# Optimization experiments

Hardware: AMD Instinct MI355X
Metric: run time of the kernel (lower is better)

## Reference

```python
import jax, jax.numpy as jnp
import numpy as np

NUM_HEADS = 8
WS = 2  # window_size


def setup_inputs() -> dict:
    key = jax.random.key(0)
    k1, k2, k3 = jax.random.split(key, 3)
    B, N, C = 8, 4096, 512
    x = jax.random.normal(k1, (B, N, C), dtype=jnp.float32)
    W_qkv = jax.random.normal(k2, (3 * C, C), dtype=jnp.float32) * 0.02  # nn.Linear weight [out,in], no bias
    W_proj = jax.random.normal(k3, (C, C), dtype=jnp.float32) * 0.02
    b_proj = jnp.zeros((C,), dtype=jnp.float32)
    return {"x": x, "W_qkv": W_qkv, "W_proj": W_proj, "b_proj": b_proj}


def _attn(q, k, v, scale):
    # q,k,v: [..., heads, T, hd]
    logits = jnp.einsum('...qd,...kd->...qk', q, k) * scale
    p = jax.nn.softmax(logits, axis=-1)
    return jnp.einsum('...qk,...kd->...qd', p, v)


def reference(x, W_qkv, W_proj, b_proj):
    B, N, C = x.shape
    H = W = int(N ** 0.5)
    nh, hd = NUM_HEADS, C // NUM_HEADS
    scale = hd ** -0.5

    # ---- hi branch: avg-pool then global attention on pooled tokens ----
    x_img = x.reshape(B, H, W, C)
    x_hi = x_img.reshape(B, H // WS, WS, W // WS, WS, C).mean(axis=(2, 4))  # [B,Hh,Wh,C]
    Hh, Wh = H // WS, W // WS
    N_hi = Hh * Wh
    x_hi = x_hi.reshape(B, N_hi, C)

    qkv_hi = (x_hi @ W_qkv.T).reshape(B, N_hi, 3, nh, hd).transpose(2, 0, 3, 1, 4)
    out_hi = _attn(qkv_hi[0], qkv_hi[1], qkv_hi[2], scale)          # [B,nh,N_hi,hd]
    out_hi = out_hi.transpose(0, 2, 1, 3).reshape(B, N_hi, C)

    # bilinear upsample (align_corners=False == half-pixel, matches jax.image.resize)
    hi_img = out_hi.reshape(B, Hh, Wh, C).transpose(0, 3, 1, 2)      # [B,C,Hh,Wh]
    hi_up = jax.image.resize(hi_img, (B, C, H, W), method='bilinear')
    out_hi = hi_up.reshape(B, C, N).transpose(0, 2, 1)               # [B,N,C]

    # ---- lo branch: windowed attention (replicating torch unfold layout) ----
    # torch: x.unfold(1,ws,ws).unfold(2,ws,ws) -> [B,Hh,Wh,C,ws,ws]; then
    # .reshape(B,-1,ws*ws,C) reinterprets the contiguous [C,ws,ws] block as [ws*ws,C].
    wnd = x_img.reshape(B, Hh, WS, Wh, WS, C).transpose(0, 1, 3, 5, 2, 4)  # [B,Hh,Wh,C,ws,ws]
    nW = Hh * Wh
    T = WS * WS
    windows = wnd.reshape(B, nW, T, C)  # same raw-memory reinterpretation as torch

    qkv_lo = (windows @ W_qkv.T).reshape(B, nW, T, 3, nh, hd).transpose(3, 0, 1, 4, 2, 5)
    out_lo = _attn(qkv_lo[0], qkv_lo[1], qkv_lo[2], scale)           # [B,nW,nh,T,hd]
    out_lo = out_lo.transpose(0, 1, 3, 2, 4).reshape(B, nW, T, C)

    out_lo = out_lo.reshape(B, Hh, Wh, WS, WS, C).transpose(0, 1, 3, 2, 4, 5).reshape(B, N, C)

    out = out_hi + out_lo
    out = out @ W_proj.T + b_proj
    return out
```

## Files before the change

kernel.cpp:

```cpp
#include <hip/hip_runtime.h>
#include <stdint.h>

typedef unsigned short u16b;
typedef short s16x8 __attribute__((ext_vector_type(8)));
typedef unsigned short u16x4 __attribute__((ext_vector_type(4)));
typedef float f32x4 __attribute__((ext_vector_type(4)));

__device__ __forceinline__ u16b f2bf(float f) {
    uint32_t u = __float_as_uint(f);
    uint32_t r = (u + 0x7FFFu + ((u >> 16) & 1u)) >> 16;
    return (u16b)r;
}
__device__ __forceinline__ u16b f2bf_fast(float f) {
    return (u16b)((__float_as_uint(f) + 0x8000u) >> 16);
}
__device__ __forceinline__ float bf2f(u16b h) {
    return __uint_as_float(((uint32_t)h) << 16);
}

typedef const __attribute__((address_space(1))) void* gas_ptr;
typedef __attribute__((address_space(3))) void* las_ptr;
__device__ __forceinline__ void gload_lds16(const void* g, void* l) {
    __builtin_amdgcn_global_load_lds((gas_ptr)g, (las_ptr)l, 16, 0, 0);
}

__global__ void cast_weights(const float* __restrict__ wqkv, const float* __restrict__ wproj,
                             u16b* __restrict__ wqkv_bf, u16b* __restrict__ wproj_bf) {
    int i = blockIdx.x * 256 + threadIdx.x;
    if (i < 1536 * 512) wqkv_bf[i] = f2bf(wqkv[i]);
    if (i < 512 * 512) wproj_bf[i] = f2bf(wproj[i]);
}

__global__ __launch_bounds__(256) void pool_pack(const float* __restrict__ x,
                                                 u16b* __restrict__ x_hi,
                                                 u16b* __restrict__ xw) {
    int i = blockIdx.x * 256 + threadIdx.x;
    int c4 = i & 127;
    int t = i >> 7;
    int wj = t & 31, wi = (t >> 5) & 31, b = t >> 10;
    const float* p00 = x + ((size_t)b * 4096 + (size_t)(wi * 2) * 64 + wj * 2) * 512 + c4 * 4;
    f32x4 v00 = *(const f32x4*)p00;
    f32x4 v01 = *(const f32x4*)(p00 + 512);
    f32x4 v10 = *(const f32x4*)(p00 + 64 * 512);
    f32x4 v11 = *(const f32x4*)(p00 + 65 * 512);

    u16b ph[4];
#pragma unroll
    for (int j = 0; j < 4; ++j)
        ph[j] = f2bf((v00[j] + v01[j] + v10[j] + v11[j]) * 0.25f);
    *(u16x4*)(x_hi + (size_t)t * 512 + c4 * 4) = *(u16x4*)ph;

    u16b pk[16];
#pragma unroll
    for (int j = 0; j < 4; ++j) {
        pk[j * 4 + 0] = f2bf(v00[j]);
        pk[j * 4 + 1] = f2bf(v01[j]);
        pk[j * 4 + 2] = f2bf(v10[j]);
        pk[j * 4 + 3] = f2bf(v11[j]);
    }
    u16b* dst = xw + ((size_t)t * 4 + (c4 >> 5)) * 512 + (c4 & 31) * 16;
    *(s16x8*)dst = *(s16x8*)pk;
    *(s16x8*)(dst + 8) = *(s16x8*)(pk + 8);
}

template <int OUT_F32>
__global__ __launch_bounds__(256) void gemm_bt(const u16b* __restrict__ A, const u16b* __restrict__ Bt,
                                               u16b* __restrict__ Cbf, float* __restrict__ Cf,
                                               const float* __restrict__ bias, int M, int Nn, int K) {
    __shared__ u16b As[128 * 64];
    __shared__ u16b Bs[128 * 64];
    int tid = threadIdx.x;
    int wave = tid >> 6, lane = tid & 63;
    int quad = lane >> 4, l15 = lane & 15;
    int m0 = blockIdx.y * 128, n0 = blockIdx.x * 128;
    int wm = (wave >> 1) * 64, wn = (wave & 1) * 64;

    f32x4 acc[4][4] = {};

    int ldrow = lane >> 3;
    int ldk = ((lane & 7) ^ ldrow) * 8;
    int fsw0 = (quad ^ (l15 & 7)) * 8;
    int fsw1 = ((4 + quad) ^ (l15 & 7)) * 8;

    for (int kc = 0; kc < K; kc += 64) {
#pragma unroll
        for (int i = 0; i < 4; ++i) {
            int chunk = wave * 4 + i;
            int row = chunk * 8 + ldrow;
            gload_lds16(A + (size_t)(m0 + row) * K + kc + ldk, As + chunk * 512);
            gload_lds16(Bt + (size_t)(n0 + row) * K + kc + ldk, Bs + chunk * 512);
        }
        __syncthreads();
#pragma unroll
        for (int ks = 0; ks < 2; ++ks) {
            int fo = ks ? fsw1 : fsw0;
            s16x8 a[4], b[4];
#pragma unroll
            for (int mi = 0; mi < 4; ++mi)
                a[mi] = *(const s16x8*)(As + (wm + mi * 16 + l15) * 64 + fo);
#pragma unroll
            for (int ni = 0; ni < 4; ++ni)
                b[ni] = *(const s16x8*)(Bs + (wn + ni * 16 + l15) * 64 + fo);
#pragma unroll
            for (int mi = 0; mi < 4; ++mi)
#pragma unroll
                for (int ni = 0; ni < 4; ++ni)
                    acc[mi][ni] = __builtin_amdgcn_mfma_f32_16x16x32_bf16(a[mi], b[ni], acc[mi][ni], 0, 0, 0);
        }
        __syncthreads();
    }

#pragma unroll
    for (int mi = 0; mi < 4; ++mi)
#pragma unroll
        for (int ni = 0; ni < 4; ++ni) {
            int row = m0 + wm + mi * 16 + quad * 4;
            int col = n0 + wn + ni * 16 + l15;
            if (OUT_F32) {
                float bv = bias[col];
#pragma unroll
                for (int r = 0; r < 4; ++r)
                    Cf[(size_t)(row + r) * Nn + col] = acc[mi][ni][r] + bv;
            } else {
#pragma unroll
                for (int r = 0; r < 4; ++r)
                    Cbf[(size_t)(row + r) * Nn + col] = f2bf(acc[mi][ni][r]);
            }
        }
}

__global__ __launch_bounds__(256) void transpose_v(const u16b* __restrict__ qkv, u16b* __restrict__ vt) {
    __shared__ u16b tile[64 * 72];
    int bh = blockIdx.y, nt = blockIdx.x;
    int b = bh >> 3, h = bh & 7;
    int tid = threadIdx.x;
    int row = tid >> 2, part = tid & 3;
    const u16b* src = qkv + ((size_t)b * 1024 + nt * 64 + row) * 1536 + 1024 + h * 64 + part * 16;
    *(s16x8*)&tile[row * 72 + part * 16] = *(const s16x8*)src;
    *(s16x8*)&tile[row * 72 + part * 16 + 8] = *(const s16x8*)(src + 8);
    __syncthreads();
    u16b* dst = vt + ((size_t)bh * 64 + row) * 1024 + nt * 64 + part * 16;
#pragma unroll
    for (int j = 0; j < 16; ++j) dst[j] = tile[(part * 16 + j) * 72 + row];
}

__global__ __launch_bounds__(256) void attn_hi(const u16b* __restrict__ qkv,
                                               const u16b* __restrict__ vt,
                                               u16b* __restrict__ out_hi) {
    __shared__ u16b Ks[2][64 * 64];
    __shared__ u16b Vs[2][64 * 64];
    __shared__ u16b P[4][16 * 64];
    int tid = threadIdx.x, wave = tid >> 6, lane = tid & 63;
    int quad = lane >> 4, l15 = lane & 15;
    int bh = blockIdx.x;
    int qb = blockIdx.y;
    int b = bh >> 3, h = bh & 7;
    int qr0 = qb * 64 + wave * 16;

    const size_t qkv_b = (size_t)b * 1024 * 1536;
    const u16b* kg = qkv + qkv_b + 512 + h * 64;
    const u16b* vg = vt + (size_t)bh * 64 * 1024;

    int srow8 = lane >> 3;
    int ssw = ((lane & 7) ^ srow8) * 8;
    int fsw0 = (quad ^ (l15 & 7)) * 8;
    int fsw1 = ((4 + quad) ^ (l15 & 7)) * 8;

    s16x8 qf[2];
    qf[0] = *(const s16x8*)(qkv + qkv_b + (size_t)(qr0 + l15) * 1536 + h * 64 + quad * 8);
    qf[1] = *(const s16x8*)(qkv + qkv_b + (size_t)(qr0 + l15) * 1536 + h * 64 + 32 + quad * 8);

#pragma unroll
    for (int i = 0; i < 2; ++i) {
        int chunk = wave * 2 + i;
        int row = chunk * 8 + srow8;
        gload_lds16(kg + (size_t)row * 1536 + ssw, (u16b*)Ks[0] + chunk * 512);
        gload_lds16(vg + (size_t)row * 1024 + ssw, (u16b*)Vs[0] + chunk * 512);
    }

    f32x4 o[4] = {};
    f32x4 ls = {0.f, 0.f, 0.f, 0.f};
    u16b* pl = P[wave];
    const float c_scale = 0.18033688011f;

    for (int kb = 0; kb < 16; ++kb) {
        int cur = kb & 1, nxt = cur ^ 1;
        __syncthreads();
        if (kb < 15) {
#pragma unroll
            for (int i = 0; i < 2; ++i) {
                int chunk = wave * 2 + i;
                int row = chunk * 8 + srow8;
                gload_lds16(kg + (size_t)((kb + 1) * 64 + row) * 1536 + ssw, (u16b*)Ks[nxt] + chunk * 512);
                gload_lds16(vg + (size_t)row * 1024 + (kb + 1) * 64 + ssw, (u16b*)Vs[nxt] + chunk * 512);
            }
        }
        const u16b* Kc = Ks[cur];
        const u16b* Vc = Vs[cur];

        f32x4 s[4] = {};
#pragma unroll
        for (int nt = 0; nt < 4; ++nt) {
            s16x8 kf0 = *(const s16x8*)(Kc + (nt * 16 + l15) * 64 + fsw0);
            s16x8 kf1 = *(const s16x8*)(Kc + (nt * 16 + l15) * 64 + fsw1);
            s[nt] = __builtin_amdgcn_mfma_f32_16x16x32_bf16(qf[0], kf0, s[nt], 0, 0, 0);
            s[nt] = __builtin_amdgcn_mfma_f32_16x16x32_bf16(qf[1], kf1, s[nt], 0, 0, 0);
        }
#pragma unroll
        for (int nt = 0; nt < 4; ++nt) {
            f32x4 p;
#pragma unroll
            for (int r = 0; r < 4; ++r) p[r] = exp2f(s[nt][r] * c_scale);
            ls += p;
#pragma unroll
            for (int r = 0; r < 4; ++r) {
                int prow = quad * 4 + r;
                int slc = (nt * 2 + (l15 >> 3)) ^ (prow & 7);
                pl[prow * 64 + slc * 8 + (l15 & 7)] = f2bf_fast(p[r]);
            }
        }
        s16x8 pa0 = *(const s16x8*)(pl + l15 * 64 + fsw0);
        s16x8 pa1 = *(const s16x8*)(pl + l15 * 64 + fsw1);
#pragma unroll
        for (int nd = 0; nd < 4; ++nd) {
            s16x8 vf0 = *(const s16x8*)(Vc + (nd * 16 + l15) * 64 + fsw0);
            s16x8 vf1 = *(const s16x8*)(Vc + (nd * 16 + l15) * 64 + fsw1);
            o[nd] = __builtin_amdgcn_mfma_f32_16x16x32_bf16(pa0, vf0, o[nd], 0, 0, 0);
            o[nd] = __builtin_amdgcn_mfma_f32_16x16x32_bf16(pa1, vf1, o[nd], 0, 0, 0);
        }
    }

    float rs[4];
#pragma unroll
    for (int r = 0; r < 4; ++r) {
        float t = ls[r];
#pragma unroll
        for (int msk = 1; msk < 16; msk <<= 1) t += __shfl_xor(t, msk);
        rs[r] = 1.f / t;
    }
#pragma unroll
    for (int nd = 0; nd < 4; ++nd)
#pragma unroll
        for (int r = 0; r < 4; ++r) {
            int row = qr0 + quad * 4 + r;
            int col = h * 64 + nd * 16 + l15;
            out_hi[((size_t)b * 1024 + row) * 512 + col] = f2bf(o[nd][r] * rs[r]);
        }
}

__global__ __launch_bounds__(256) void attn_lo_up(const u16b* __restrict__ qkv_lo,
                                                  const u16b* __restrict__ out_hi,
                                                  u16b* __restrict__ attn_sum) {
    int tid = threadIdx.x, wave = tid >> 6, lane = tid & 63;
    int wg = blockIdx.x * 4 + wave;
    int h = wg & 7, w = (wg >> 3) & 1023, b = wg >> 13;
    size_t base = ((size_t)(b * 1024 + w) * 4) * 1536 + h * 64 + lane;
    float q[4], k[4], v[4];
#pragma unroll
    for (int t = 0; t < 4; ++t) {
        q[t] = bf2f(qkv_lo[base + t * 1536]);
        k[t] = bf2f(qkv_lo[base + t * 1536 + 512]);
        v[t] = bf2f(qkv_lo[base + t * 1536 + 1024]);
    }
    float lg[4][4];
#pragma unroll
    for (int tq = 0; tq < 4; ++tq)
#pragma unroll
        for (int tk = 0; tk < 4; ++tk) {
            float d = q[tq] * k[tk];
#pragma unroll
            for (int msk = 1; msk < 64; msk <<= 1) d += __shfl_xor(d, msk);
            lg[tq][tk] = d * 0.125f;
        }
    int wi = w >> 5, wj = w & 31;
    const u16b* hsrc = out_hi + (size_t)b * 1024 * 512 + h * 64 + lane;
#pragma unroll
    for (int tq = 0; tq < 4; ++tq) {
        float mx = fmaxf(fmaxf(lg[tq][0], lg[tq][1]), fmaxf(lg[tq][2], lg[tq][3]));
        float p[4], s = 0.f;
#pragma unroll
        for (int tk = 0; tk < 4; ++tk) { p[tk] = exp2f((lg[tq][tk] - mx) * 1.44269504f); s += p[tk]; }
        float ov = 0.f;
#pragma unroll
        for (int tk = 0; tk < 4; ++tk) ov += p[tk] * v[tk];
        ov /= s;
        int py = tq >> 1, px = tq & 1;
        int y0, y1, x0, x1;
        float wy0, wx0;
        if (py == 0) { y0 = wi > 0 ? wi - 1 : 0; y1 = wi; wy0 = 0.25f; }
        else         { y0 = wi; y1 = wi < 31 ? wi + 1 : 31; wy0 = 0.75f; }
        if (px == 0) { x0 = wj > 0 ? wj - 1 : 0; x1 = wj; wx0 = 0.25f; }
        else         { x0 = wj; x1 = wj < 31 ? wj + 1 : 31; wx0 = 0.75f; }
        float wy1 = 1.f - wy0, wx1 = 1.f - wx0;
        float vu = wy0 * (wx0 * bf2f(hsrc[(size_t)(y0 * 32 + x0) * 512]) + wx1 * bf2f(hsrc[(size_t)(y0 * 32 + x1) * 512]))
                 + wy1 * (wx0 * bf2f(hsrc[(size_t)(y1 * 32 + x0) * 512]) + wx1 * bf2f(hsrc[(size_t)(y1 * 32 + x1) * 512]));
        int n = (wi * 2 + py) * 64 + wj * 2 + px;
        attn_sum[((size_t)b * 4096 + n) * 512 + h * 64 + lane] = f2bf(ov + vu);
    }
}

extern "C" void kernel_launch(void* const* d_in, const int* in_sizes, int n_in,
                              void* d_out, int out_size, void* d_ws, size_t ws_size,
                              hipStream_t stream) {
    (void)in_sizes; (void)n_in; (void)out_size; (void)ws_size;
    const float* x = (const float*)d_in[0];
    const float* Wqkv = (const float*)d_in[1];
    const float* Wproj = (const float*)d_in[2];
    const float* bproj = (const float*)d_in[3];
    float* out = (float*)d_out;

    char* ws = (char*)d_ws;
    size_t off = 0;
    auto alloc = [&](size_t bytes) { void* p = ws + off; off += bytes; return p; };
    u16b* wqkv_bf = (u16b*)alloc((size_t)1536 * 512 * 2);
    u16b* wproj_bf = (u16b*)alloc((size_t)512 * 512 * 2);
    u16b* x_hi    = (u16b*)alloc((size_t)8 * 1024 * 512 * 2);
    u16b* xw      = (u16b*)alloc((size_t)8 * 1024 * 4 * 512 * 2);
    u16b* qkv_hi  = (u16b*)alloc((size_t)8 * 1024 * 1536 * 2);
    u16b* qkv_lo  = (u16b*)alloc((size_t)8 * 4096 * 1536 * 2);
    u16b* vt      = (u16b*)alloc((size_t)64 * 64 * 1024 * 2);
    u16b* out_hi  = (u16b*)alloc((size_t)8 * 1024 * 512 * 2);
    u16b* attn_sum= (u16b*)alloc((size_t)8 * 4096 * 512 * 2);

    cast_weights<<<dim3(3072), dim3(256), 0, stream>>>(Wqkv, Wproj, wqkv_bf, wproj_bf);
    pool_pack<<<dim3(4096), dim3(256), 0, stream>>>(x, x_hi, xw);
    gemm_bt<0><<<dim3(12, 64), dim3(256), 0, stream>>>(x_hi, wqkv_bf, qkv_hi, nullptr, nullptr, 8192, 1536, 512);
    gemm_bt<0><<<dim3(12, 256), dim3(256), 0, stream>>>(xw, wqkv_bf, qkv_lo, nullptr, nullptr, 32768, 1536, 512);
    transpose_v<<<dim3(16, 64), dim3(256), 0, stream>>>(qkv_hi, vt);
    attn_hi<<<dim3(64, 16), dim3(256), 0, stream>>>(qkv_hi, vt, out_hi);
    attn_lo_up<<<dim3(16384), dim3(256), 0, stream>>>(qkv_lo, out_hi, attn_sum);
    gemm_bt<1><<<dim3(4, 256), dim3(256), 0, stream>>>(attn_sum, wproj_bf, nullptr, out, bproj, 32768, 512, 512);
}
```

Baseline: 350.8 us.

## Replace GEMM with 256x256 double-buffered 8-wave pipelined kernel

```diff
diff --git a/kernel.cpp b/kernel.cpp
--- a/kernel.cpp
+++ b/kernel.cpp
@@ -63,59 +63,154 @@
     *(s16x8*)(dst + 8) = *(s16x8*)(pk + 8);
 }
 
+
+template <int RT>
+__device__ __forceinline__ void stage_region(const u16b* gsrc, int K, u16b* lds,
+                                             int wv, int ldrow, int ldk) {
+#pragma unroll
+    for (int j = 0; j < 2; ++j) {
+        int c = j * 8 + wv;
+        int chunk;
+        if (RT == 0)      chunk = c + ((c >> 3) << 3);
+        else if (RT == 1) chunk = c + ((c >> 3) << 3) + 8;
+        else if (RT == 2) chunk = ((c >> 2) << 3) + (c & 3);
+        else              chunk = ((c >> 2) << 3) + (c & 3) + 4;
+        gload_lds16(gsrc + (size_t)(chunk * 8 + ldrow) * K + ldk, lds + chunk * 512);
+    }
+}
+
+template <int MH, int NH, int LOADB>
+__device__ __forceinline__ void ds_quad(const u16b* Asb, const u16b* Bsb,
+                                        int gm, int gn, int l15, int fsw0, int fsw1,
+                                        s16x8 (&af)[4][2], s16x8 (&bf)[2][2]) {
+#pragma unroll
+    for (int i = 0; i < 4; ++i) {
+        const u16b* p = Asb + (gm * 128 + (MH * 4 + i) * 16 + l15) * 64;
+        af[i][0] = *(const s16x8*)(p + fsw0);
+        af[i][1] = *(const s16x8*)(p + fsw1);
+    }
+    if (LOADB) {
+#pragma unroll
+        for (int i = 0; i < 2; ++i) {
+            const u16b* p = Bsb + (gn * 64 + (NH * 2 + i) * 16 + l15) * 64;
+            bf[i][0] = *(const s16x8*)(p + fsw0);
+            bf[i][1] = *(const s16x8*)(p + fsw1);
+        }
+    }
+}
+
+template <int MH, int NH>
+__device__ __forceinline__ void mfma_quad(s16x8 (&af)[4][2], s16x8 (&bf)[2][2], f32x4 (&acc)[8][4]) {
+    __builtin_amdgcn_s_setprio(1);
+#pragma unroll
+    for (int ks = 0; ks < 2; ++ks)
+#pragma unroll
+        for (int i = 0; i < 4; ++i)
+#pragma unroll
+            for (int j = 0; j < 2; ++j)
+                acc[MH * 4 + i][NH * 2 + j] = __builtin_amdgcn_mfma_f32_16x16x32_bf16(
+                    af[i][ks], bf[j][ks], acc[MH * 4 + i][NH * 2 + j], 0, 0, 0);
+    __builtin_amdgcn_s_setprio(0);
+}
+
 template <int OUT_F32>
-__global__ __launch_bounds__(256) void gemm_bt(const u16b* __restrict__ A, const u16b* __restrict__ Bt,
-                                               u16b* __restrict__ Cbf, float* __restrict__ Cf,
-                                               const float* __restrict__ bias, int M, int Nn, int K) {
-    __shared__ u16b As[128 * 64];
-    __shared__ u16b Bs[128 * 64];
+__global__ __launch_bounds__(512, 2) void gemm8(const u16b* __restrict__ A, const u16b* __restrict__ Bt,
+                                                u16b* __restrict__ Cbf, float* __restrict__ Cf,
+                                                const float* __restrict__ bias, int M, int Nn, int K,
+                                                int NB) {
+    __shared__ u16b As[2][256 * 64];
+    __shared__ u16b Bs[2][256 * 64];
     int tid = threadIdx.x;
-    int wave = tid >> 6, lane = tid & 63;
+    int wv = tid >> 6, lane = tid & 63;
     int quad = lane >> 4, l15 = lane & 15;
-    int m0 = blockIdx.y * 128, n0 = blockIdx.x * 128;
-    int wm = (wave >> 1) * 64, wn = (wave & 1) * 64;
-
-    f32x4 acc[4][4] = {};
+    int gm = wv >> 2, gn = wv & 3;
+
+    int nwg = gridDim.x, bid = blockIdx.x;
+    int swz = (bid & 7) * (nwg >> 3) + (bid >> 3);
+    int nb = swz % NB, mb = swz / NB;
+    int m0 = mb * 256, n0 = nb * 256;
+    const u16b* Ap = A + (size_t)m0 * K;
+    const u16b* Btp = Bt + (size_t)n0 * K;
 
     int ldrow = lane >> 3;
     int ldk = ((lane & 7) ^ ldrow) * 8;
     int fsw0 = (quad ^ (l15 & 7)) * 8;
     int fsw1 = ((4 + quad) ^ (l15 & 7)) * 8;
 
-    for (int kc = 0; kc < K; kc += 64) {
-#pragma unroll
-        for (int i = 0; i < 4; ++i) {
-            int chunk = wave * 4 + i;
-            int row = chunk * 8 + ldrow;
-            gload_lds16(A + (size_t)(m0 + row) * K + kc + ldk, As + chunk * 512);
-            gload_lds16(Bt + (size_t)(n0 + row) * K + kc + ldk, Bs + chunk * 512);
-        }
-        __syncthreads();
-#pragma unroll
-        for (int ks = 0; ks < 2; ++ks) {
-            int fo = ks ? fsw1 : fsw0;
-            s16x8 a[4], b[4];
-#pragma unroll
-            for (int mi = 0; mi < 4; ++mi)
-                a[mi] = *(const s16x8*)(As + (wm + mi * 16 + l15) * 64 + fo);
-#pragma unroll
-            for (int ni = 0; ni < 4; ++ni)
-                b[ni] = *(const s16x8*)(Bs + (wn + ni * 16 + l15) * 64 + fo);
-#pragma unroll
-            for (int mi = 0; mi < 4; ++mi)
-#pragma unroll
-                for (int ni = 0; ni < 4; ++ni)
-                    acc[mi][ni] = __builtin_amdgcn_mfma_f32_16x16x32_bf16(a[mi], b[ni], acc[mi][ni], 0, 0, 0);
-        }
-        __syncthreads();
-    }
-
-#pragma unroll
-    for (int mi = 0; mi < 4; ++mi)
+    f32x4 acc[8][4] = {};
+    s16x8 af[4][2], bf[2][2];
+    int nt = K >> 6;
+
+#pragma unroll
+    for (int r = 0; r < 4; ++r) {
+        int chunk = r * 8 + wv;
+        gload_lds16(Ap + (size_t)(chunk * 8 + ldrow) * K + ldk, &As[0][0] + chunk * 512);
+    }
+#pragma unroll
+    for (int r = 0; r < 4; ++r) {
+        int chunk = r * 8 + wv;
+        gload_lds16(Btp + (size_t)(chunk * 8 + ldrow) * K + ldk, &Bs[0][0] + chunk * 512);
+    }
+    stage_region<2>(Btp + 64, K, &Bs[1][0], wv, ldrow, ldk);
+    stage_region<0>(Ap + 64, K, &As[1][0], wv, ldrow, ldk);
+    asm volatile("s_waitcnt vmcnt(4)" ::: "memory");
+    __builtin_amdgcn_s_barrier();
+
+    for (int t0 = 0; t0 < nt; t0 += 2) {
+        bool s2 = (t0 + 2) < nt;
+        bool s3 = (t0 + 3) < nt;
+        ds_quad<0, 0, 1>(&As[0][0], &Bs[0][0], gm, gn, l15, fsw0, fsw1, af, bf);
+        stage_region<3>(Btp + (size_t)(t0 + 1) * 64, K, &Bs[1][0], wv, ldrow, ldk);
+        __builtin_amdgcn_s_barrier();
+        mfma_quad<0, 0>(af, bf, acc);
+        __builtin_amdgcn_s_barrier();
+        ds_quad<1, 0, 0>(&As[0][0], &Bs[0][0], gm, gn, l15, fsw0, fsw1, af, bf);
+        stage_region<1>(Ap + (size_t)(t0 + 1) * 64, K, &As[1][0], wv, ldrow, ldk);
+        __builtin_amdgcn_s_barrier();
+        mfma_quad<1, 0>(af, bf, acc);
+        __builtin_amdgcn_s_barrier();
+        ds_quad<0, 1, 1>(&As[0][0], &Bs[0][0], gm, gn, l15, fsw0, fsw1, af, bf);
+        if (s2) stage_region<2>(Btp + (size_t)(t0 + 2) * 64, K, &Bs[0][0], wv, ldrow, ldk);
+        __builtin_amdgcn_s_barrier();
+        mfma_quad<0, 1>(af, bf, acc);
+        __builtin_amdgcn_s_barrier();
+        ds_quad<1, 1, 0>(&As[0][0], &Bs[0][0], gm, gn, l15, fsw0, fsw1, af, bf);
+        if (s2) stage_region<0>(Ap + (size_t)(t0 + 2) * 64, K, &As[0][0], wv, ldrow, ldk);
+        __builtin_amdgcn_s_barrier();
+        mfma_quad<1, 1>(af, bf, acc);
+        if (s2) { asm volatile("s_waitcnt vmcnt(4)" ::: "memory"); }
+        else    { asm volatile("s_waitcnt vmcnt(0)" ::: "memory"); }
+        __builtin_amdgcn_s_barrier();
+        ds_quad<0, 0, 1>(&As[1][0], &Bs[1][0], gm, gn, l15, fsw0, fsw1, af, bf);
+        if (s2) stage_region<3>(Btp + (size_t)(t0 + 2) * 64, K, &Bs[0][0], wv, ldrow, ldk);
+        __builtin_amdgcn_s_barrier();
+        mfma_quad<0, 0>(af, bf, acc);
+        __builtin_amdgcn_s_barrier();
+        ds_quad<1, 0, 0>(&As[1][0], &Bs[1][0], gm, gn, l15, fsw0, fsw1, af, bf);
+        if (s2) stage_region<1>(Ap + (size_t)(t0 + 2) * 64, K, &As[0][0], wv, ldrow, ldk);
+        __builtin_amdgcn_s_barrier();
+        mfma_quad<1, 0>(af, bf, acc);
+        __builtin_amdgcn_s_barrier();
+        ds_quad<0, 1, 1>(&As[1][0], &Bs[1][0], gm, gn, l15, fsw0, fsw1, af, bf);
+        if (s3) stage_region<2>(Btp + (size_t)(t0 + 3) * 64, K, &Bs[1][0], wv, ldrow, ldk);
+        __builtin_amdgcn_s_barrier();
+        mfma_quad<0, 1>(af, bf, acc);
+        __builtin_amdgcn_s_barrier();
+        ds_quad<1, 1, 0>(&As[1][0], &Bs[1][0], gm, gn, l15, fsw0, fsw1, af, bf);
+        if (s3) stage_region<0>(Ap + (size_t)(t0 + 3) * 64, K, &As[1][0], wv, ldrow, ldk);
+        __builtin_amdgcn_s_barrier();
+        mfma_quad<1, 1>(af, bf, acc);
+        if (s3) { asm volatile("s_waitcnt vmcnt(4)" ::: "memory"); }
+        else    { asm volatile("s_waitcnt vmcnt(0)" ::: "memory"); }
+        __builtin_amdgcn_s_barrier();
+    }
+
+#pragma unroll
+    for (int mi = 0; mi < 8; ++mi)
 #pragma unroll
         for (int ni = 0; ni < 4; ++ni) {
-            int row = m0 + wm + mi * 16 + quad * 4;
-            int col = n0 + wn + ni * 16 + l15;
+            int row = m0 + gm * 128 + mi * 16 + quad * 4;
+            int col = n0 + gn * 64 + ni * 16 + l15;
             if (OUT_F32) {
                 float bv = bias[col];
 #pragma unroll
@@ -324,10 +419,10 @@
 
     cast_weights<<<dim3(3072), dim3(256), 0, stream>>>(Wqkv, Wproj, wqkv_bf, wproj_bf);
     pool_pack<<<dim3(4096), dim3(256), 0, stream>>>(x, x_hi, xw);
-    gemm_bt<0><<<dim3(12, 64), dim3(256), 0, stream>>>(x_hi, wqkv_bf, qkv_hi, nullptr, nullptr, 8192, 1536, 512);
-    gemm_bt<0><<<dim3(12, 256), dim3(256), 0, stream>>>(xw, wqkv_bf, qkv_lo, nullptr, nullptr, 32768, 1536, 512);
+    gemm8<0><<<dim3(192), dim3(512), 0, stream>>>(x_hi, wqkv_bf, qkv_hi, nullptr, nullptr, 8192, 1536, 512, 6);
+    gemm8<0><<<dim3(768), dim3(512), 0, stream>>>(xw, wqkv_bf, qkv_lo, nullptr, nullptr, 32768, 1536, 512, 6);
     transpose_v<<<dim3(16, 64), dim3(256), 0, stream>>>(qkv_hi, vt);
     attn_hi<<<dim3(64, 16), dim3(256), 0, stream>>>(qkv_hi, vt, out_hi);
     attn_lo_up<<<dim3(16384), dim3(256), 0, stream>>>(qkv_lo, out_hi, attn_sum);
-    gemm_bt<1><<<dim3(4, 256), dim3(256), 0, stream>>>(attn_sum, wproj_bf, nullptr, out, bproj, 32768, 512, 512);
-}
+    gemm8<1><<<dim3(256), dim3(512), 0, stream>>>(attn_sum, wproj_bf, nullptr, out, bproj, 32768, 512, 512, 2);
+}
```

New measurement: 356.2 us. No clear change (+1.5%).
